# Kernel optimization log

Measured on AMD Instinct MI355X. Metric: run time of the kernel, lower is better.

## Reference

```python
import jax, jax.numpy as jnp
import numpy as np

EPS = 1e-5  # matches module default eps


def setup_inputs() -> dict:
    key = jax.random.key(0)
    n, F = 4096, 256
    k1, k2, k3, k4, k5 = jax.random.split(key, 5)
    # Orthonormal eigenbasis (eigh of a symmetric Laplacian yields orthogonal V)
    V = jnp.linalg.qr(jax.random.normal(k1, (n, n), dtype=jnp.float32))[0]
    # Nonnegative Laplacian spectrum with lam[0] = 0 (module asserts sqrtlam[0] ~ 0)
    lam = jnp.sort(jax.random.uniform(k2, (n,), dtype=jnp.float32) * 4.0)
    lam = lam.at[0].set(0.0)
    x = jax.random.normal(k3, (n, F, 1), dtype=jnp.float32)
    y = jax.random.normal(k4, (n, F, 1), dtype=jnp.float32)
    t = jnp.float32(0.7)
    return {"x": x, "y": y, "t": t, "lam": lam, "V": V}


def reference(x, y, t, lam, V):
    # safe_sqrt: clamp tiny negatives (|lam|<eps) to zero before sqrt
    sqrtlam = jnp.sqrt(jnp.maximum(lam, 0.0))
    # P1 spectrum: cos(t * sqrt(lam))
    c = jnp.cos(t * sqrtlam)
    # P2 spectrum: sin(t*s)/s with limit t as s->0 (safe_P2_eigh)
    small = jnp.abs(sqrtlam) < EPS
    safe_s = jnp.where(small, 1.0, sqrtlam)
    p2 = jnp.where(small, t, jnp.sin(t * safe_s) / safe_s)

    def apply_spectral(d, sig):
        # (V diag(d) V^T) @ sig, contracted over node axis; sig: [n, F, C]
        vt_sig = jnp.einsum('ji,jfc->ifc', V, sig)          # V^T @ sig
        return jnp.einsum('ij,jfc->ifc', V, d[:, None, None] * vt_sig)

    # res1 + res2: P1 @ x + P2 @ y (the scatter-add message passing with all
    # nonzeros of the dense P matrices is exactly this dense mat-vec)
    return apply_spectral(c, x) + apply_spectral(p2, y)
```

## Files before the change

### kernel.cpp

```cpp
#include <hip/hip_runtime.h>

typedef __attribute__((ext_vector_type(8))) short short8;
typedef __attribute__((ext_vector_type(8))) unsigned short ushort8v;
typedef __attribute__((ext_vector_type(4))) float f32x4;

#define N_NODES 4096
#define N_FEAT  256

__device__ __forceinline__ unsigned short f2bf(float f) {
  union { float f; unsigned u; } a; a.f = f;
  unsigned r = a.u + 0x7FFFu + ((a.u >> 16) & 1u);
  return (unsigned short)(r >> 16);
}

__device__ __forceinline__ void gload_lds16(const void* g, void* l) {
  __builtin_amdgcn_global_load_lds(
      (const __attribute__((address_space(1))) void*)g,
      (__attribute__((address_space(3))) void*)l, 16, 0, 0);
}

__global__ void spectrum_k(const float* __restrict__ lam, const float* __restrict__ tp,
                           float* __restrict__ cbuf, float* __restrict__ p2buf) {
  int i = blockIdx.x * 256 + threadIdx.x;
  float tv = tp[0];
  float s = sqrtf(fmaxf(lam[i], 0.f));
  cbuf[i] = cosf(tv * s);
  p2buf[i] = (s < 1e-5f) ? tv : (sinf(tv * s) / s);
}

__global__ __launch_bounds__(256) void prep_v_k(const float* __restrict__ V,
                                                unsigned short* __restrict__ Vbf,
                                                unsigned short* __restrict__ Vt) {
  __shared__ unsigned short tile[64][72];
  const int t = threadIdx.x;
  const int r = t >> 2, q = t & 3;
  const int gr = blockIdx.y * 64 + r;
  const int gc0 = blockIdx.x * 64;
#pragma unroll
  for (int i = 0; i < 4; ++i) {
    int c = q * 4 + i * 16;
    float4 v = *(const float4*)&V[(size_t)gr * N_NODES + gc0 + c];
    ushort4 u; u.x = f2bf(v.x); u.y = f2bf(v.y); u.z = f2bf(v.z); u.w = f2bf(v.w);
    *(ushort4*)&Vbf[(size_t)gr * N_NODES + gc0 + c] = u;
    tile[c + 0][r] = u.x; tile[c + 1][r] = u.y; tile[c + 2][r] = u.z; tile[c + 3][r] = u.w;
  }
  __syncthreads();
  const int r2 = t >> 2;
#pragma unroll
  for (int j = 0; j < 2; ++j) {
    int ms = q * 8 + j * 32;
    ushort8v u = *(const ushort8v*)&tile[r2][ms];
    *(ushort8v*)&Vt[(size_t)(gc0 + r2) * N_NODES + blockIdx.y * 64 + ms] = u;
  }
}

__global__ __launch_bounds__(256) void prep_xy_k(const float* __restrict__ x,
                                                 const float* __restrict__ y,
                                                 unsigned short* __restrict__ S2T) {
  __shared__ unsigned short tx[64][72];
  __shared__ unsigned short ty[64][72];
  const int t = threadIdx.x;
  const int r = t >> 2, q = t & 3;
  const int gj = blockIdx.y * 64 + r;
  const int gf0 = blockIdx.x * 64;
#pragma unroll
  for (int i = 0; i < 4; ++i) {
    int c = q * 4 + i * 16;
    float4 vx = *(const float4*)&x[(size_t)gj * N_FEAT + gf0 + c];
    float4 vy = *(const float4*)&y[(size_t)gj * N_FEAT + gf0 + c];
    tx[c + 0][r] = f2bf(vx.x); tx[c + 1][r] = f2bf(vx.y);
    tx[c + 2][r] = f2bf(vx.z); tx[c + 3][r] = f2bf(vx.w);
    ty[c + 0][r] = f2bf(vy.x); ty[c + 1][r] = f2bf(vy.y);
    ty[c + 2][r] = f2bf(vy.z); ty[c + 3][r] = f2bf(vy.w);
  }
  __syncthreads();
  const int f2 = t >> 2;
#pragma unroll
  for (int j = 0; j < 2; ++j) {
    int js = q * 8 + j * 32;
    ushort8v ux = *(const ushort8v*)&tx[f2][js];
    ushort8v uy = *(const ushort8v*)&ty[f2][js];
    *(ushort8v*)&S2T[(size_t)(2 * (gf0 + f2) + 0) * N_NODES + blockIdx.y * 64 + js] = ux;
    *(ushort8v*)&S2T[(size_t)(2 * (gf0 + f2) + 1) * N_NODES + blockIdx.y * 64 + js] = uy;
  }
}

template <int NTB>
__global__ __launch_bounds__(256, 4) void gemm_swz(const unsigned short* __restrict__ A,
                                                   const unsigned short* __restrict__ B,
                                                   float* __restrict__ part,
                                                   int K, int Kc, int Nn, size_t MN) {
  __shared__ unsigned short As[128 * 64];
  __shared__ unsigned short Bs[64 * 64];
  const int t = threadIdx.x;
  const int lane = t & 63, w = t >> 6;

  const unsigned L = blockIdx.x;
  const unsigned cx = L & 7u, j = L >> 3;
  const unsigned ntile = j & ((1u << NTB) - 1u);
  const unsigned group = cx * (128u >> NTB) + (j >> NTB);
  const unsigned mtile = group & 31u;
  const unsigned zz = group >> 5u;

  const int wr = (w >> 1) * 64;
  const int wc = (w & 1) * 32;
  const int l15 = lane & 15;
  const int lhi = lane >> 4;

  const size_t kbase = (size_t)zz * Kc;
  const size_t srcoff = (size_t)(lane >> 3) * K * 2 + (size_t)(((lane & 7) ^ (lane >> 3)) << 4);

  const char* Ag = (const char*)(A + (size_t)mtile * 128 * K + kbase);
  const char* Bg = (const char*)(B + (size_t)ntile * 64 * K + kbase);

  f32x4 acc[4][2];
#pragma unroll
  for (int mi = 0; mi < 4; ++mi)
#pragma unroll
    for (int ni = 0; ni < 2; ++ni) acc[mi][ni] = (f32x4){0.f, 0.f, 0.f, 0.f};

  const int nkt = Kc >> 6;
  for (int kt = 0; kt < nkt; ++kt) {
    const size_t ko = (size_t)kt * 128;
#pragma unroll
    for (int q = 0; q < 4; ++q)
      gload_lds16(Ag + (size_t)(w * 4 + q) * 8 * K * 2 + srcoff + ko, &As[(w * 4 + q) * 512]);
#pragma unroll
    for (int q = 0; q < 2; ++q)
      gload_lds16(Bg + (size_t)(w * 2 + q) * 8 * K * 2 + srcoff + ko, &Bs[(w * 2 + q) * 512]);
    __syncthreads();
    short8 a[4][2], b[2][2];
#pragma unroll
    for (int mi = 0; mi < 4; ++mi) {
      const int ar = wr + mi * 16 + l15;
#pragma unroll
      for (int ks = 0; ks < 2; ++ks)
        a[mi][ks] = *(const short8*)((const char*)As + (size_t)ar * 128 +
                                     ((((ks << 2) | lhi) ^ (ar & 7)) << 4));
    }
#pragma unroll
    for (int ni = 0; ni < 2; ++ni) {
      const int br = wc + ni * 16 + l15;
#pragma unroll
      for (int ks = 0; ks < 2; ++ks)
        b[ni][ks] = *(const short8*)((const char*)Bs + (size_t)br * 128 +
                                     ((((ks << 2) | lhi) ^ (br & 7)) << 4));
    }
#pragma unroll
    for (int ks = 0; ks < 2; ++ks)
#pragma unroll
      for (int mi = 0; mi < 4; ++mi)
#pragma unroll
        for (int ni = 0; ni < 2; ++ni)
          acc[mi][ni] = __builtin_amdgcn_mfma_f32_16x16x32_bf16(a[mi][ks], b[ni][ks],
                                                                acc[mi][ni], 0, 0, 0);
    __syncthreads();
  }

  float* po = part + (size_t)zz * MN;
  const int m0 = mtile * 128 + wr + lhi * 4;
  const int n0 = ntile * 64 + wc + l15;
#pragma unroll
  for (int mi = 0; mi < 4; ++mi)
#pragma unroll
    for (int ni = 0; ni < 2; ++ni)
#pragma unroll
      for (int r = 0; r < 4; ++r)
        po[(size_t)(m0 + mi * 16 + r) * Nn + n0 + ni * 16] = acc[mi][ni][r];
}

__global__ __launch_bounds__(256) void reduce1_k(const float* __restrict__ part,
                                                 const float* __restrict__ cbuf,
                                                 const float* __restrict__ p2buf,
                                                 unsigned short* __restrict__ Zt) {
  __shared__ unsigned short zt[64][72];
  const int t = threadIdx.x;
  const int r = t >> 2, q = t & 3;
  const int m = blockIdx.y * 64 + r;
  const int n0 = blockIdx.x * 128;
  const float cv = cbuf[m], pv = p2buf[m];
  float acc[16];
#pragma unroll
  for (int i = 0; i < 16; ++i) acc[i] = 0.f;
  for (int ks = 0; ks < 4; ++ks) {
    const float* p = part + ((size_t)ks * N_NODES + m) * 512 + n0;
#pragma unroll
    for (int i = 0; i < 8; ++i) {
      float4 v = *(const float4*)&p[q * 4 + i * 16];
      acc[2 * i + 0] += cv * v.x + pv * v.y;
      acc[2 * i + 1] += cv * v.z + pv * v.w;
    }
  }
#pragma unroll
  for (int i = 0; i < 8; ++i) {
    int f = q * 2 + i * 8;
    zt[f + 0][r] = f2bf(acc[2 * i + 0]);
    zt[f + 1][r] = f2bf(acc[2 * i + 1]);
  }
  __syncthreads();
  const int f2 = t >> 2;
  const int gf = blockIdx.x * 64 + f2;
#pragma unroll
  for (int w = 0; w < 2; ++w) {
    int js = q * 8 + w * 32;
    ushort8v u = *(const ushort8v*)&zt[f2][js];
    *(ushort8v*)&Zt[(size_t)gf * N_NODES + blockIdx.y * 64 + js] = u;
  }
}

__global__ __launch_bounds__(256) void reduce2_k(const float* __restrict__ part,
                                                 float* __restrict__ out) {
  const size_t e = ((size_t)blockIdx.x * 256 + threadIdx.x) * 4;
  float4 s = {0.f, 0.f, 0.f, 0.f};
#pragma unroll
  for (int ks = 0; ks < 8; ++ks) {
    float4 v = *(const float4*)&part[(size_t)ks * N_NODES * N_FEAT + e];
    s.x += v.x; s.y += v.y; s.z += v.z; s.w += v.w;
  }
  *(float4*)&out[e] = s;
}

extern "C" void kernel_launch(void* const* d_in, const int* in_sizes, int n_in,
                              void* d_out, int out_size, void* d_ws, size_t ws_size,
                              hipStream_t stream) {
  const float* x   = (const float*)d_in[0];
  const float* y   = (const float*)d_in[1];
  const float* tp  = (const float*)d_in[2];
  const float* lam = (const float*)d_in[3];
  const float* V   = (const float*)d_in[4];

  char* w = (char*)d_ws;
  unsigned short* Vbf  = (unsigned short*)w; w += (size_t)N_NODES * N_NODES * 2;
  unsigned short* Vtbf = (unsigned short*)w; w += (size_t)N_NODES * N_NODES * 2;
  unsigned short* S2T  = (unsigned short*)w; w += (size_t)512 * N_NODES * 2;
  unsigned short* Zt   = (unsigned short*)w; w += (size_t)N_FEAT * N_NODES * 2;
  float* cbuf  = (float*)w; w += N_NODES * 4;
  float* p2buf = (float*)w; w += N_NODES * 4;
  float* partb = (float*)w; w += (size_t)4 * N_NODES * 512 * 4;

  spectrum_k<<<N_NODES / 256, 256, 0, stream>>>(lam, tp, cbuf, p2buf);
  prep_v_k<<<dim3(N_NODES / 64, N_NODES / 64), 256, 0, stream>>>(V, Vbf, Vtbf);
  prep_xy_k<<<dim3(N_FEAT / 64, N_NODES / 64), 256, 0, stream>>>(x, y, S2T);
  gemm_swz<3><<<1024, 256, 0, stream>>>(Vtbf, S2T, partb, N_NODES, 1024, 512,
                                        (size_t)N_NODES * 512);
  reduce1_k<<<dim3(512 / 128, N_NODES / 64), 256, 0, stream>>>(partb, cbuf, p2buf, Zt);
  gemm_swz<2><<<1024, 256, 0, stream>>>(Vbf, Zt, partb, N_NODES, 512, N_FEAT,
                                        (size_t)N_NODES * N_FEAT);
  reduce2_k<<<(N_NODES * N_FEAT) / 1024, 256, 0, stream>>>(partb, (float*)d_out);
}
```

Before: 178.4 us.

## Double-buffer GEMM LDS tiles, store bf16 split-K partials, fuse spectrum into reduce

The GEMM kernel now uses two LDS buffers per operand, so the next k-tile's global-to-LDS loads are issued while the current tile is multiplied, and occupancy is lowered from 4 to 3 blocks per CU to make room. Split-K partial sums are written and read as bf16 instead of fp32, halving partial-buffer traffic in both GEMMs and both reduce kernels, at some cost in accuracy. The spectrum computation is folded into reduce1, which removes one launch and two small buffers.

Measured after the change: 192.6 us. +7.9%, slower.

```diff
diff --git a/kernel.cpp b/kernel.cpp
--- a/kernel.cpp
+++ b/kernel.cpp
@@ -13,19 +13,15 @@
   return (unsigned short)(r >> 16);
 }
 
+__device__ __forceinline__ float bf2f(unsigned short u) {
+  union { unsigned u; float f; } a; a.u = ((unsigned)u) << 16;
+  return a.f;
+}
+
 __device__ __forceinline__ void gload_lds16(const void* g, void* l) {
   __builtin_amdgcn_global_load_lds(
       (const __attribute__((address_space(1))) void*)g,
       (__attribute__((address_space(3))) void*)l, 16, 0, 0);
-}
-
-__global__ void spectrum_k(const float* __restrict__ lam, const float* __restrict__ tp,
-                           float* __restrict__ cbuf, float* __restrict__ p2buf) {
-  int i = blockIdx.x * 256 + threadIdx.x;
-  float tv = tp[0];
-  float s = sqrtf(fmaxf(lam[i], 0.f));
-  cbuf[i] = cosf(tv * s);
-  p2buf[i] = (s < 1e-5f) ? tv : (sinf(tv * s) / s);
 }
 
 __global__ __launch_bounds__(256) void prep_v_k(const float* __restrict__ V,
@@ -86,12 +82,12 @@
 }
 
 template <int NTB>
-__global__ __launch_bounds__(256, 4) void gemm_swz(const unsigned short* __restrict__ A,
+__global__ __launch_bounds__(256, 3) void gemm_swz(const unsigned short* __restrict__ A,
                                                    const unsigned short* __restrict__ B,
-                                                   float* __restrict__ part,
+                                                   unsigned short* __restrict__ part,
                                                    int K, int Kc, int Nn, size_t MN) {
-  __shared__ unsigned short As[128 * 64];
-  __shared__ unsigned short Bs[64 * 64];
+  __shared__ unsigned short As[2][128 * 64];
+  __shared__ unsigned short Bs[2][64 * 64];
   const int t = threadIdx.x;
   const int lane = t & 63, w = t >> 6;
 
@@ -119,23 +115,26 @@
 #pragma unroll
     for (int ni = 0; ni < 2; ++ni) acc[mi][ni] = (f32x4){0.f, 0.f, 0.f, 0.f};
 
-  const int nkt = Kc >> 6;
-  for (int kt = 0; kt < nkt; ++kt) {
+  auto STAGE = [&](int kt, int cur) {
     const size_t ko = (size_t)kt * 128;
 #pragma unroll
     for (int q = 0; q < 4; ++q)
-      gload_lds16(Ag + (size_t)(w * 4 + q) * 8 * K * 2 + srcoff + ko, &As[(w * 4 + q) * 512]);
+      gload_lds16(Ag + (size_t)(w * 4 + q) * 8 * K * 2 + srcoff + ko,
+                  &As[cur][(w * 4 + q) * 512]);
 #pragma unroll
     for (int q = 0; q < 2; ++q)
-      gload_lds16(Bg + (size_t)(w * 2 + q) * 8 * K * 2 + srcoff + ko, &Bs[(w * 2 + q) * 512]);
-    __syncthreads();
+      gload_lds16(Bg + (size_t)(w * 2 + q) * 8 * K * 2 + srcoff + ko,
+                  &Bs[cur][(w * 2 + q) * 512]);
+  };
+
+  auto COMPUTE = [&](int cur) {
     short8 a[4][2], b[2][2];
 #pragma unroll
     for (int mi = 0; mi < 4; ++mi) {
       const int ar = wr + mi * 16 + l15;
 #pragma unroll
       for (int ks = 0; ks < 2; ++ks)
-        a[mi][ks] = *(const short8*)((const char*)As + (size_t)ar * 128 +
+        a[mi][ks] = *(const short8*)((const char*)&As[cur][0] + (size_t)ar * 128 +
                                      ((((ks << 2) | lhi) ^ (ar & 7)) << 4));
     }
 #pragma unroll
@@ -143,7 +142,7 @@
       const int br = wc + ni * 16 + l15;
 #pragma unroll
       for (int ks = 0; ks < 2; ++ks)
-        b[ni][ks] = *(const short8*)((const char*)Bs + (size_t)br * 128 +
+        b[ni][ks] = *(const short8*)((const char*)&Bs[cur][0] + (size_t)br * 128 +
                                      ((((ks << 2) | lhi) ^ (br & 7)) << 4));
     }
 #pragma unroll
@@ -154,10 +153,21 @@
         for (int ni = 0; ni < 2; ++ni)
           acc[mi][ni] = __builtin_amdgcn_mfma_f32_16x16x32_bf16(a[mi][ks], b[ni][ks],
                                                                 acc[mi][ni], 0, 0, 0);
+  };
+
+  const int nkt = Kc >> 6;
+  STAGE(0, 0);
+  __syncthreads();
+  int cur = 0;
+  for (int kt = 0; kt < nkt - 1; ++kt) {
+    STAGE(kt + 1, cur ^ 1);
+    COMPUTE(cur);
     __syncthreads();
-  }
-
-  float* po = part + (size_t)zz * MN;
+    cur ^= 1;
+  }
+  COMPUTE(cur);
+
+  unsigned short* po = part + (size_t)zz * MN;
   const int m0 = mtile * 128 + wr + lhi * 4;
   const int n0 = ntile * 64 + wc + l15;
 #pragma unroll
@@ -166,29 +176,32 @@
     for (int ni = 0; ni < 2; ++ni)
 #pragma unroll
       for (int r = 0; r < 4; ++r)
-        po[(size_t)(m0 + mi * 16 + r) * Nn + n0 + ni * 16] = acc[mi][ni][r];
-}
-
-__global__ __launch_bounds__(256) void reduce1_k(const float* __restrict__ part,
-                                                 const float* __restrict__ cbuf,
-                                                 const float* __restrict__ p2buf,
+        po[(size_t)(m0 + mi * 16 + r) * Nn + n0 + ni * 16] = f2bf(acc[mi][ni][r]);
+}
+
+__global__ __launch_bounds__(256) void reduce1_k(const unsigned short* __restrict__ part,
+                                                 const float* __restrict__ lam,
+                                                 const float* __restrict__ tp,
                                                  unsigned short* __restrict__ Zt) {
   __shared__ unsigned short zt[64][72];
   const int t = threadIdx.x;
   const int r = t >> 2, q = t & 3;
   const int m = blockIdx.y * 64 + r;
   const int n0 = blockIdx.x * 128;
-  const float cv = cbuf[m], pv = p2buf[m];
+  const float tv = tp[0];
+  const float s = sqrtf(fmaxf(lam[m], 0.f));
+  const float cv = cosf(tv * s);
+  const float pv = (s < 1e-5f) ? tv : (sinf(tv * s) / s);
   float acc[16];
 #pragma unroll
   for (int i = 0; i < 16; ++i) acc[i] = 0.f;
   for (int ks = 0; ks < 4; ++ks) {
-    const float* p = part + ((size_t)ks * N_NODES + m) * 512 + n0;
+    const unsigned short* p = part + ((size_t)ks * N_NODES + m) * 512 + n0;
 #pragma unroll
     for (int i = 0; i < 8; ++i) {
-      float4 v = *(const float4*)&p[q * 4 + i * 16];
-      acc[2 * i + 0] += cv * v.x + pv * v.y;
-      acc[2 * i + 1] += cv * v.z + pv * v.w;
+      ushort4 u = *(const ushort4*)&p[q * 4 + i * 16];
+      acc[2 * i + 0] += cv * bf2f(u.x) + pv * bf2f(u.y);
+      acc[2 * i + 1] += cv * bf2f(u.z) + pv * bf2f(u.w);
     }
   }
 #pragma unroll
@@ -208,14 +221,14 @@
   }
 }
 
-__global__ __launch_bounds__(256) void reduce2_k(const float* __restrict__ part,
+__global__ __launch_bounds__(256) void reduce2_k(const unsigned short* __restrict__ part,
                                                  float* __restrict__ out) {
   const size_t e = ((size_t)blockIdx.x * 256 + threadIdx.x) * 4;
   float4 s = {0.f, 0.f, 0.f, 0.f};
 #pragma unroll
   for (int ks = 0; ks < 8; ++ks) {
-    float4 v = *(const float4*)&part[(size_t)ks * N_NODES * N_FEAT + e];
-    s.x += v.x; s.y += v.y; s.z += v.z; s.w += v.w;
+    ushort4 u = *(const ushort4*)&part[(size_t)ks * N_NODES * N_FEAT + e];
+    s.x += bf2f(u.x); s.y += bf2f(u.y); s.z += bf2f(u.z); s.w += bf2f(u.w);
   }
   *(float4*)&out[e] = s;
 }
@@ -234,16 +247,13 @@
   unsigned short* Vtbf = (unsigned short*)w; w += (size_t)N_NODES * N_NODES * 2;
   unsigned short* S2T  = (unsigned short*)w; w += (size_t)512 * N_NODES * 2;
   unsigned short* Zt   = (unsigned short*)w; w += (size_t)N_FEAT * N_NODES * 2;
-  float* cbuf  = (float*)w; w += N_NODES * 4;
-  float* p2buf = (float*)w; w += N_NODES * 4;
-  float* partb = (float*)w; w += (size_t)4 * N_NODES * 512 * 4;
-
-  spectrum_k<<<N_NODES / 256, 256, 0, stream>>>(lam, tp, cbuf, p2buf);
+  unsigned short* partb = (unsigned short*)w; w += (size_t)4 * N_NODES * 512 * 2;
+
   prep_v_k<<<dim3(N_NODES / 64, N_NODES / 64), 256, 0, stream>>>(V, Vbf, Vtbf);
   prep_xy_k<<<dim3(N_FEAT / 64, N_NODES / 64), 256, 0, stream>>>(x, y, S2T);
   gemm_swz<3><<<1024, 256, 0, stream>>>(Vtbf, S2T, partb, N_NODES, 1024, 512,
                                         (size_t)N_NODES * 512);
-  reduce1_k<<<dim3(512 / 128, N_NODES / 64), 256, 0, stream>>>(partb, cbuf, p2buf, Zt);
+  reduce1_k<<<dim3(512 / 128, N_NODES / 64), 256, 0, stream>>>(partb, lam, tp, Zt);
   gemm_swz<2><<<1024, 256, 0, stream>>>(Vbf, Zt, partb, N_NODES, 512, N_FEAT,
                                         (size_t)N_NODES * N_FEAT);
   reduce2_k<<<(N_NODES * N_FEAT) / 1024, 256, 0, stream>>>(partb, (float*)d_out);
```
